# Performance work log

Hardware: AMD Instinct MI355X
Metric: run time of the kernel (lower is better)

Reference implementation:

```python
import jax, jax.numpy as jnp
import numpy as np

D_MODEL, D_HID, N_EXPERTS, TOP_K = 1024, 4096, 8, 2

def setup_inputs() -> dict:
    key = jax.random.key(0)
    ks = jax.random.split(key, 6)
    B, T = 2, 2048
    x = jax.random.normal(ks[0], (B, T, D_MODEL), dtype=jnp.float32)
    gate_w = jax.random.normal(ks[1], (N_EXPERTS, D_MODEL), dtype=jnp.float32) * (1.0 / np.sqrt(D_MODEL))
    # kaiming_uniform-ish init for expert weights
    lim1 = np.sqrt(6.0 / D_MODEL)
    lim2 = np.sqrt(6.0 / D_HID)
    w1 = jax.random.uniform(ks[2], (N_EXPERTS, D_MODEL, D_HID), dtype=jnp.float32, minval=-lim1, maxval=lim1)
    w2 = jax.random.uniform(ks[3], (N_EXPERTS, D_HID, D_MODEL), dtype=jnp.float32, minval=-lim2, maxval=lim2)
    b1 = jnp.zeros((N_EXPERTS, 1, D_HID), dtype=jnp.float32)
    b2 = jnp.zeros((N_EXPERTS, 1, D_MODEL), dtype=jnp.float32)
    return {"x": x, "gate_w": gate_w, "w1": w1, "b1": b1, "w2": w2, "b2": b2}

def reference(x, gate_w, w1, b1, w2, b2):
    B, T, D = x.shape
    E = gate_w.shape[0]
    xf = x.reshape(-1, D)                              # [N, D]
    N = xf.shape[0]
    # Router: logits -> softmax -> top-k -> renormalize
    logits = jnp.einsum('nd,ed->ne', xf, gate_w)       # [N, E]
    scores = jax.nn.softmax(logits, axis=-1)
    top_w, top_i = jax.lax.top_k(scores, TOP_K)        # [N, K]
    top_w = top_w / jnp.sum(top_w, axis=-1, keepdims=True)
    # Dense combine weights (zero for unselected experts) — same math as
    # the padded-bmm dispatch/combine: padded slots have weight 0.
    gates = jnp.zeros((N, E), xf.dtype).at[jnp.arange(N)[:, None], top_i].add(top_w)  # [N, E]
    # Grouped expert MLP (computed densely; weighted combine zeroes unrouted experts)
    h = jax.nn.gelu(jnp.einsum('nd,edh->enh', xf, w1) + b1, approximate=False)  # [E, N, H]
    expert_out = jnp.einsum('enh,ehd->end', h, w2) + b2                          # [E, N, D]
    out = jnp.einsum('end,ne->nd', expert_out, gates)                            # [N, D]
    return out.reshape(B, T, D)
```

## Files before the change

### kernel.cpp

```cpp
#include <hip/hip_runtime.h>
#include <math.h>

#define NTOK 4096
#define DM   1024
#define DH   4096
#define NE   8
#define NSLOT (NTOK*2)

typedef unsigned short u16;
typedef __attribute__((ext_vector_type(8))) short shortx8;
typedef __attribute__((ext_vector_type(4))) float floatx4;
typedef __attribute__((ext_vector_type(4))) int   intx4;

__device__ __forceinline__ u16 f2bf(float f) {
  union { float f; unsigned u; } c; c.f = f;
  unsigned r = c.u + 0x7fffu + ((c.u >> 16) & 1u);
  return (u16)(r >> 16);
}

__device__ __forceinline__ void async_cp16(const u16* g, u16* l) {
  __builtin_amdgcn_global_load_lds(
      (const __attribute__((address_space(1))) void*)g,
      (__attribute__((address_space(3))) void*)l, 16, 0, 0);
}

__global__ void cvt_x_kernel(const float* __restrict__ x, u16* __restrict__ xb) {
  int i = (blockIdx.x * 256 + threadIdx.x) * 8;
  float4 v0 = *(const float4*)(x + i);
  float4 v1 = *(const float4*)(x + i + 4);
  u16 tmp[8] = {f2bf(v0.x), f2bf(v0.y), f2bf(v0.z), f2bf(v0.w),
                f2bf(v1.x), f2bf(v1.y), f2bf(v1.z), f2bf(v1.w)};
  *(intx4*)(xb + i) = *(intx4*)tmp;
}

template<int K, int NW>
__global__ void transpose_kernel(const float* __restrict__ W, u16* __restrict__ Wt) {
  int e = blockIdx.z;
  const float* Wp = W + (size_t)e * K * NW;
  u16* Wtp = Wt + (size_t)e * K * NW;
  int n = blockIdx.x * 64 + (threadIdx.x & 63);
  int kend = blockIdx.y * 256 + 256;
  for (int k0 = blockIdx.y * 256 + (threadIdx.x >> 6) * 8; k0 < kend; k0 += 32) {
    u16 tmp[8];
#pragma unroll
    for (int j = 0; j < 8; j++) tmp[j] = f2bf(Wp[(size_t)(k0 + j) * NW + n]);
    *(intx4*)(Wtp + (size_t)n * K + k0) = *(intx4*)tmp;
  }
}

__global__ __launch_bounds__(256) void router_kernel(const float* __restrict__ x,
                                                     const float* __restrict__ gw,
                                                     int* __restrict__ eos,
                                                     float* __restrict__ wos) {
  int wave = threadIdx.x >> 6, lane = threadIdx.x & 63;
  int n = blockIdx.x * 4 + wave;
  const float* xr = x + (size_t)n * DM;
  float acc[NE];
#pragma unroll
  for (int e = 0; e < NE; e++) acc[e] = 0.f;
  for (int d = lane; d < DM; d += 64) {
    float xv = xr[d];
#pragma unroll
    for (int e = 0; e < NE; e++) acc[e] += xv * gw[e * DM + d];
  }
#pragma unroll
  for (int e = 0; e < NE; e++) {
    float v = acc[e];
#pragma unroll
    for (int off = 32; off > 0; off >>= 1) v += __shfl_xor(v, off, 64);
    acc[e] = v;
  }
  if (lane == 0) {
    int i0 = 0;
    for (int e = 1; e < NE; e++) if (acc[e] > acc[i0]) i0 = e;
    int i1 = (i0 == 0) ? 1 : 0;
    for (int e = 0; e < NE; e++) { if (e == i0) continue; if (acc[e] > acc[i1]) i1 = e; }
    float e1 = expf(acc[i1] - acc[i0]);
    float w0 = 1.f / (1.f + e1);
    eos[2 * n] = i0;  eos[2 * n + 1] = i1;
    wos[2 * n] = w0;  wos[2 * n + 1] = 1.f - w0;
  }
}

__global__ __launch_bounds__(256) void build_groups_kernel(
    const int* __restrict__ eos, const float* __restrict__ wos,
    int* __restrict__ goff, int* __restrict__ tok_of_g, float* __restrict__ w_of_g) {
  __shared__ int pref[256][NE];
  __shared__ int tot[NE];
  __shared__ int ebase[NE + 1];
  int t = threadIdx.x;
  int c[NE];
#pragma unroll
  for (int e = 0; e < NE; e++) c[e] = 0;
  for (int i = 0; i < NSLOT / 256; i++) {
    int e = eos[t * (NSLOT / 256) + i];
#pragma unroll
    for (int q = 0; q < NE; q++) if (e == q) c[q]++;
  }
#pragma unroll
  for (int e = 0; e < NE; e++) pref[t][e] = c[e];
  __syncthreads();
  if (t < NE) {
    int run = 0;
    for (int i = 0; i < 256; i++) { int v = pref[i][t]; pref[i][t] = run; run += v; }
    tot[t] = run;
  }
  __syncthreads();
  if (t == 0) {
    int o = 0;
    for (int e = 0; e < NE; e++) { ebase[e] = o; o += tot[e]; }
    ebase[NE] = o;
  }
  __syncthreads();
  int off[NE];
#pragma unroll
  for (int e = 0; e < NE; e++) off[e] = ebase[e] + pref[t][e];
  for (int i = 0; i < NSLOT / 256; i++) {
    int s = t * (NSLOT / 256) + i;
    int e = eos[s];
    int g = 0;
#pragma unroll
    for (int q = 0; q < NE; q++) if (e == q) { g = off[q]; off[q] = g + 1; }
    tok_of_g[g] = s >> 1;
    w_of_g[g] = wos[s];
  }
  if (t <= NE) goff[t] = ebase[t];
}

template<int K, int NOUT, int MODE>
__global__ __launch_bounds__(256) void moe_gemm(
    const u16* __restrict__ A, const u16* __restrict__ Wt, const float* __restrict__ bias,
    const int* __restrict__ goff, const int* __restrict__ tok_of_g,
    const float* __restrict__ w_of_g,
    u16* __restrict__ Hout, float* __restrict__ Out) {
  int e = blockIdx.z;
  int gb = goff[e];
  int cntE = goff[e + 1] - gb;
  int m0 = blockIdx.y * 128;
  if (m0 >= cntE) return;
  int mvalid = cntE - m0; if (mvalid > 128) mvalid = 128;
  int gbase = gb + m0;
  int n0 = blockIdx.x * 128;
  int tid = threadIdx.x;
  int lane = tid & 63, wave = tid >> 6;

  __shared__ __align__(16) u16 As[128 * 32];
  __shared__ __align__(16) u16 Bs[128 * 32];

  int sr = lane >> 2;
  int sc = (lane & 3) * 8;
  int ra0 = wave * 16 + sr;
  int ra1 = 64 + wave * 16 + sr;
  int ca0 = (ra0 < mvalid) ? ra0 : (mvalid - 1);
  int ca1 = (ra1 < mvalid) ? ra1 : (mvalid - 1);
  const u16 *pa0, *pa1;
  if (MODE == 0) {
    pa0 = A + (size_t)tok_of_g[gbase + ca0] * K + sc;
    pa1 = A + (size_t)tok_of_g[gbase + ca1] * K + sc;
  } else {
    pa0 = A + (size_t)(gbase + ca0) * K + sc;
    pa1 = A + (size_t)(gbase + ca1) * K + sc;
  }
  const u16* wte = Wt + (size_t)e * NOUT * K;
  const u16* pb0 = wte + (size_t)(n0 + ra0) * K + sc;
  const u16* pb1 = wte + (size_t)(n0 + ra1) * K + sc;
  u16* ldsA0 = As + wave * 512;
  u16* ldsA1 = As + 2048 + wave * 512;
  u16* ldsB0 = Bs + wave * 512;
  u16* ldsB1 = Bs + 2048 + wave * 512;

  int wm = wave >> 1, wn = wave & 1;
  int lr = lane & 15, lk = (lane >> 4) * 8;

  floatx4 acc[4][4];
#pragma unroll
  for (int i = 0; i < 4; i++)
#pragma unroll
    for (int j = 0; j < 4; j++) acc[i][j] = (floatx4){0.f, 0.f, 0.f, 0.f};

  for (int k0 = 0; k0 < K; k0 += 32) {
    __syncthreads();
    async_cp16(pa0 + k0, ldsA0);
    async_cp16(pa1 + k0, ldsA1);
    async_cp16(pb0 + k0, ldsB0);
    async_cp16(pb1 + k0, ldsB1);
    __syncthreads();
    shortx8 af[4], bfr[4];
#pragma unroll
    for (int i = 0; i < 4; i++) {
      af[i]  = *(const shortx8*)&As[(wm * 64 + i * 16 + lr) * 32 + lk];
      bfr[i] = *(const shortx8*)&Bs[(wn * 64 + i * 16 + lr) * 32 + lk];
    }
#pragma unroll
    for (int i = 0; i < 4; i++)
#pragma unroll
      for (int j = 0; j < 4; j++)
        acc[i][j] = __builtin_amdgcn_mfma_f32_16x16x32_bf16(af[i], bfr[j], acc[i][j], 0, 0, 0);
  }

  const float* bp = bias + (size_t)e * NOUT + n0;
  if (MODE == 0) {
#pragma unroll
    for (int i = 0; i < 4; i++) {
      int rowb = wm * 64 + i * 16 + (lane >> 4) * 4;
#pragma unroll
      for (int r = 0; r < 4; r++) {
        int grow = rowb + r;
        if (grow < mvalid) {
          size_t base = (size_t)(gbase + grow) * NOUT + n0;
#pragma unroll
          for (int j = 0; j < 4; j++) {
            int col = wn * 64 + j * 16 + lr;
            float v = acc[i][j][r] + bp[col];
            v = 0.5f * v * (1.f + erff(v * 0.70710678118654752f));
            Hout[base + col] = f2bf(v);
          }
        }
      }
    }
  } else {
#pragma unroll
    for (int i = 0; i < 4; i++) {
      int rowb = wm * 64 + i * 16 + (lane >> 4) * 4;
#pragma unroll
      for (int r = 0; r < 4; r++) {
        int grow = rowb + r;
        if (grow < mvalid) {
          int gi = gbase + grow;
          int t = tok_of_g[gi];
          float wg = w_of_g[gi];
          float* orow = Out + (size_t)t * DM + n0;
#pragma unroll
          for (int j = 0; j < 4; j++) {
            int col = wn * 64 + j * 16 + lr;
            atomicAdd(&orow[col], wg * (acc[i][j][r] + bp[col]));
          }
        }
      }
    }
  }
}

extern "C" void kernel_launch(void* const* d_in, const int* in_sizes, int n_in,
                              void* d_out, int out_size, void* d_ws, size_t ws_size,
                              hipStream_t stream) {
  const float* x  = (const float*)d_in[0];
  const float* gw = (const float*)d_in[1];
  const float* w1 = (const float*)d_in[2];
  const float* b1 = (const float*)d_in[3];
  const float* w2 = (const float*)d_in[4];
  const float* b2 = (const float*)d_in[5];
  float* out = (float*)d_out;
  char* ws = (char*)d_ws;

  u16* xb = (u16*)(ws + 0);
  u16* wt = (u16*)(ws + 8388608);
  u16* h  = (u16*)(ws + 75497472);
  char* meta = ws + 142606336;
  int*   eos      = (int*)(meta);
  int*   tok_of_g = (int*)(meta + 32768);
  float* wos      = (float*)(meta + 65536);
  float* w_of_g   = (float*)(meta + 98304);
  int*   goff     = (int*)(meta + 131072);

  hipMemsetAsync(out, 0, (size_t)NTOK * DM * 4, stream);

  cvt_x_kernel<<<NTOK * DM / 8 / 256, 256, 0, stream>>>(x, xb);
  transpose_kernel<DM, DH><<<dim3(DH / 64, DM / 256, NE), 256, 0, stream>>>(w1, wt);
  router_kernel<<<NTOK / 4, 256, 0, stream>>>(x, gw, eos, wos);
  build_groups_kernel<<<1, 256, 0, stream>>>(eos, wos, goff, tok_of_g, w_of_g);
  moe_gemm<DM, DH, 0><<<dim3(DH / 128, NTOK / 128, NE), 256, 0, stream>>>(
      xb, wt, b1, goff, tok_of_g, w_of_g, h, nullptr);
  transpose_kernel<DH, DM><<<dim3(DM / 64, DH / 256, NE), 256, 0, stream>>>(w2, wt);
  moe_gemm<DH, DM, 1><<<dim3(DM / 128, NTOK / 128, NE), 256, 0, stream>>>(
      h, wt, b2, goff, tok_of_g, w_of_g, nullptr, out);
}
```

Measured before the change: 693.4 us.

## Double-buffer LDS tiles, interleave experts in grid, split-K the down projection

```diff
diff --git a/kernel.cpp b/kernel.cpp
--- a/kernel.cpp
+++ b/kernel.cpp
@@ -127,25 +127,33 @@
   if (t <= NE) goff[t] = ebase[t];
 }
 
-template<int K, int NOUT, int MODE>
+template<int K, int NOUT, int MODE, int KSPLIT>
 __global__ __launch_bounds__(256) void moe_gemm(
     const u16* __restrict__ A, const u16* __restrict__ Wt, const float* __restrict__ bias,
     const int* __restrict__ goff, const int* __restrict__ tok_of_g,
     const float* __restrict__ w_of_g,
     u16* __restrict__ Hout, float* __restrict__ Out) {
-  int e = blockIdx.z;
+  const int KLEN = K / KSPLIT;
+  int id = blockIdx.x;
+  int e = id & 7;
+  int s = id >> 3;
+  int kseg = 0;
+  if (KSPLIT > 1) { kseg = s & (KSPLIT - 1); s >>= 1; }
+  int mb = s & 31;
+  int nb = s >> 5;
   int gb = goff[e];
   int cntE = goff[e + 1] - gb;
-  int m0 = blockIdx.y * 128;
+  int m0 = mb * 128;
   if (m0 >= cntE) return;
   int mvalid = cntE - m0; if (mvalid > 128) mvalid = 128;
   int gbase = gb + m0;
-  int n0 = blockIdx.x * 128;
+  int n0 = nb * 128;
+  int kbeg = kseg * KLEN;
   int tid = threadIdx.x;
   int lane = tid & 63, wave = tid >> 6;
 
-  __shared__ __align__(16) u16 As[128 * 32];
-  __shared__ __align__(16) u16 Bs[128 * 32];
+  __shared__ __align__(16) u16 As0[128 * 32], Bs0[128 * 32];
+  __shared__ __align__(16) u16 As1[128 * 32], Bs1[128 * 32];
 
   int sr = lane >> 2;
   int sc = (lane & 3) * 8;
@@ -164,10 +172,7 @@
   const u16* wte = Wt + (size_t)e * NOUT * K;
   const u16* pb0 = wte + (size_t)(n0 + ra0) * K + sc;
   const u16* pb1 = wte + (size_t)(n0 + ra1) * K + sc;
-  u16* ldsA0 = As + wave * 512;
-  u16* ldsA1 = As + 2048 + wave * 512;
-  u16* ldsB0 = Bs + wave * 512;
-  u16* ldsB1 = Bs + 2048 + wave * 512;
+  int ldso = wave * 512;
 
   int wm = wave >> 1, wn = wave & 1;
   int lr = lane & 15, lk = (lane >> 4) * 8;
@@ -178,25 +183,45 @@
 #pragma unroll
     for (int j = 0; j < 4; j++) acc[i][j] = (floatx4){0.f, 0.f, 0.f, 0.f};
 
-  for (int k0 = 0; k0 < K; k0 += 32) {
+#define STAGE(k0, AS, BS)                    \
+  do {                                       \
+    async_cp16(pa0 + (k0), AS + ldso);       \
+    async_cp16(pa1 + (k0), AS + 2048 + ldso);\
+    async_cp16(pb0 + (k0), BS + ldso);       \
+    async_cp16(pb1 + (k0), BS + 2048 + ldso);\
+  } while (0)
+
+#define COMPUTE(AS, BS)                                                         \
+  do {                                                                          \
+    shortx8 af[4], bfr[4];                                                      \
+    _Pragma("unroll")                                                           \
+    for (int i = 0; i < 4; i++) {                                               \
+      af[i]  = *(const shortx8*)&AS[(wm * 64 + i * 16 + lr) * 32 + lk];         \
+      bfr[i] = *(const shortx8*)&BS[(wn * 64 + i * 16 + lr) * 32 + lk];         \
+    }                                                                           \
+    _Pragma("unroll")                                                           \
+    for (int i = 0; i < 4; i++)                                                 \
+      _Pragma("unroll")                                                         \
+      for (int j = 0; j < 4; j++)                                               \
+        acc[i][j] = __builtin_amdgcn_mfma_f32_16x16x32_bf16(af[i], bfr[j],      \
+                                                            acc[i][j], 0, 0, 0);\
+  } while (0)
+
+  STAGE(kbeg, As0, Bs0);
+  __syncthreads();
+  int k0 = kbeg;
+  for (; k0 + 64 < kbeg + KLEN; k0 += 64) {
+    STAGE(k0 + 32, As1, Bs1);
+    COMPUTE(As0, Bs0);
     __syncthreads();
-    async_cp16(pa0 + k0, ldsA0);
-    async_cp16(pa1 + k0, ldsA1);
-    async_cp16(pb0 + k0, ldsB0);
-    async_cp16(pb1 + k0, ldsB1);
+    STAGE(k0 + 64, As0, Bs0);
+    COMPUTE(As1, Bs1);
     __syncthreads();
-    shortx8 af[4], bfr[4];
-#pragma unroll
-    for (int i = 0; i < 4; i++) {
-      af[i]  = *(const shortx8*)&As[(wm * 64 + i * 16 + lr) * 32 + lk];
-      bfr[i] = *(const shortx8*)&Bs[(wn * 64 + i * 16 + lr) * 32 + lk];
-    }
-#pragma unroll
-    for (int i = 0; i < 4; i++)
-#pragma unroll
-      for (int j = 0; j < 4; j++)
-        acc[i][j] = __builtin_amdgcn_mfma_f32_16x16x32_bf16(af[i], bfr[j], acc[i][j], 0, 0, 0);
-  }
+  }
+  STAGE(k0 + 32, As1, Bs1);
+  COMPUTE(As0, Bs0);
+  __syncthreads();
+  COMPUTE(As1, Bs1);
 
   const float* bp = bias + (size_t)e * NOUT + n0;
   if (MODE == 0) {
@@ -233,12 +258,15 @@
 #pragma unroll
           for (int j = 0; j < 4; j++) {
             int col = wn * 64 + j * 16 + lr;
-            atomicAdd(&orow[col], wg * (acc[i][j][r] + bp[col]));
+            float bb = (kseg == 0) ? bp[col] : 0.f;
+            atomicAdd(&orow[col], wg * (acc[i][j][r] + bb));
           }
         }
       }
     }
   }
+#undef STAGE
+#undef COMPUTE
 }
 
 extern "C" void kernel_launch(void* const* d_in, const int* in_sizes, int n_in,
@@ -269,9 +297,9 @@
   transpose_kernel<DM, DH><<<dim3(DH / 64, DM / 256, NE), 256, 0, stream>>>(w1, wt);
   router_kernel<<<NTOK / 4, 256, 0, stream>>>(x, gw, eos, wos);
   build_groups_kernel<<<1, 256, 0, stream>>>(eos, wos, goff, tok_of_g, w_of_g);
-  moe_gemm<DM, DH, 0><<<dim3(DH / 128, NTOK / 128, NE), 256, 0, stream>>>(
+  moe_gemm<DM, DH, 0, 1><<<NE * 32 * 32, 256, 0, stream>>>(
       xb, wt, b1, goff, tok_of_g, w_of_g, h, nullptr);
   transpose_kernel<DH, DM><<<dim3(DM / 64, DH / 256, NE), 256, 0, stream>>>(w2, wt);
-  moe_gemm<DH, DM, 1><<<dim3(DM / 128, NTOK / 128, NE), 256, 0, stream>>>(
+  moe_gemm<DH, DM, 1, 2><<<NE * 8 * 2 * 32, 256, 0, stream>>>(
       h, wt, b2, goff, tok_of_g, w_of_g, nullptr, out);
 }
```

After: 806.0 us. 1.16x slower.
